# Optimization experiments

Hardware: AMD Instinct MI355X
Metric: run time of the kernel (lower is better)

Reference implementation:

```python
import jax, jax.numpy as jnp
import numpy as np

EPS = 1e-5
NEG = -1e9

def rmsnorm(x, g, eps=EPS):
    x32 = x.astype(jnp.float32)
    n = x32 * jax.lax.rsqrt(jnp.mean(x32 * x32, axis=-1, keepdims=True) + eps)
    return g * n.astype(x.dtype)

def setup_inputs() -> dict:
    key = jax.random.key(0)
    ks = jax.random.split(key, 10)
    B, S, D, H = 2, 2048, 768, 12
    F = 4 * D
    s = 0.02
    return {
        "x": jax.random.normal(ks[0], (B, S, D), jnp.float32),
        "mask": jax.random.randint(ks[1], (B, S, S), 0, 2, jnp.int32),
        "wq": jax.random.normal(ks[2], (D, D), jnp.float32) * s,
        "wk": jax.random.normal(ks[3], (D, D), jnp.float32) * s,
        "wv": jax.random.normal(ks[4], (D, D), jnp.float32) * s,
        "wo": jax.random.normal(ks[5], (D, D), jnp.float32) * s,
        "w1": jax.random.normal(ks[6], (F, D), jnp.float32) * s,
        "w2": jax.random.normal(ks[7], (D, F), jnp.float32) * s,
        "w3": jax.random.normal(ks[8], (F, D), jnp.float32) * s,
        "g_attn": jnp.ones((D,), jnp.float32),
        "g_ffn": jnp.ones((D,), jnp.float32),
    }

def reference(x, mask, wq, wk, wv, wo, w1, w2, w3, g_attn, g_ffn):
    B, S, D = x.shape
    H = 12
    Dk = D // H
    # --- attention sub-block (pre-norm) ---
    xn = rmsnorm(x, g_attn)
    # torch Linear: y = x @ W^T; split heads -> [B,H,S,Dk]
    q = (xn @ wq.T).reshape(B, S, H, Dk).transpose(0, 2, 1, 3)
    k = (xn @ wk.T).reshape(B, S, H, Dk).transpose(0, 2, 1, 3)
    v = (xn @ wv.T).reshape(B, S, H, Dk).transpose(0, 2, 1, 3)
    scores = jnp.einsum("bhqd,bhkd->bhqk", q, k) / jnp.sqrt(jnp.float32(Dk))
    scores = jnp.where(mask[:, None, :, :] == 0, jnp.float32(NEG), scores)
    probs = jax.nn.softmax(scores, axis=-1)  # dropout p=0.0 -> identity
    attn = jnp.einsum("bhqk,bhkd->bhqd", probs, v)
    attn = attn.transpose(0, 2, 1, 3).reshape(B, S, D)
    h = x + attn @ wo.T
    # --- SwiGLU FFN sub-block (pre-norm) ---
    hn = rmsnorm(h, g_ffn)
    ffn = (jax.nn.silu(hn @ w1.T) * (hn @ w3.T)) @ w2.T
    return h + ffn
```

## Files before the change

### kernel.cpp

```cpp
#include <hip/hip_runtime.h>
#include <hip/hip_bf16.h>

#define S_LEN 2048
#define D_MODEL 768
#define NH 12
#define DK 64
#define F_DIM 3072
#define BATCH 2
#define M_ROWS (BATCH * S_LEN)

typedef __bf16 bf16x8 __attribute__((ext_vector_type(8)));
typedef float floatx4 __attribute__((ext_vector_type(4)));
typedef unsigned short u16;
typedef unsigned long long u64;

__device__ inline float bf2f(u16 u) {
    union { unsigned int i; float f; } x; x.i = ((unsigned int)u) << 16; return x.f;
}
__device__ inline u16 f2bf(float f) {
    union { float f; unsigned int i; } x; x.f = f;
    unsigned int r = x.i + 0x7fffu + ((x.i >> 16) & 1u);
    return (u16)(r >> 16);
}

__device__ __forceinline__ void ldsload16(const u16* g, u16* l) {
    __builtin_amdgcn_global_load_lds(
        (const __attribute__((address_space(1))) unsigned int*)g,
        (__attribute__((address_space(3))) unsigned int*)l, 16, 0, 0);
}

__global__ __launch_bounds__(256)
void cvt_all(const float4* __restrict__ wq, const float4* __restrict__ wk,
             const float4* __restrict__ wv, const float4* __restrict__ wo,
             const float4* __restrict__ w1, const float4* __restrict__ w2,
             const float4* __restrict__ w3,
             ushort4* wqb, ushort4* wkb, ushort4* wvb, ushort4* wob,
             ushort4* w1b, ushort4* w2b, ushort4* w3b) {
    const int WS4 = (D_MODEL * D_MODEL) / 4;
    const int WB4 = (F_DIM * D_MODEL) / 4;
    int i = blockIdx.x * 256 + threadIdx.x;
    const float4* src; ushort4* dst; int off;
    if (i < 4 * WS4) {
        int s = i / WS4; off = i - s * WS4;
        src = (s == 0) ? wq : (s == 1) ? wk : (s == 2) ? wv : wo;
        dst = (s == 0) ? wqb : (s == 1) ? wkb : (s == 2) ? wvb : wob;
    } else {
        int j = i - 4 * WS4; int s = j / WB4; off = j - s * WB4;
        src = (s == 0) ? w1 : (s == 1) ? w2 : w3;
        dst = (s == 0) ? w1b : (s == 1) ? w2b : w3b;
    }
    float4 v = src[off];
    ushort4 o;
    o.x = f2bf(v.x); o.y = f2bf(v.y); o.z = f2bf(v.z); o.w = f2bf(v.w);
    dst[off] = o;
}

__global__ __launch_bounds__(256)
void mask_bits(const int* __restrict__ m, u64* __restrict__ bits) {
    size_t gid = (size_t)blockIdx.x * 256 + threadIdx.x;
    u64 b = __ballot(m[gid] != 0);
    if ((threadIdx.x & 63) == 0) bits[gid >> 6] = b;
}

__global__ __launch_bounds__(256)
void rmsnorm_k(const float* __restrict__ x, const float* __restrict__ g, u16* __restrict__ out) {
    int row = blockIdx.x;
    const float* xr = x + (size_t)row * D_MODEL;
    u16* orow = out + (size_t)row * D_MODEL;
    int t = threadIdx.x;
    float v0 = xr[t];
    float v1 = xr[t + 256];
    float v2 = xr[t + 512];
    float ss = v0 * v0 + v1 * v1 + v2 * v2;
    #pragma unroll
    for (int off = 1; off < 64; off <<= 1) ss += __shfl_xor(ss, off);
    __shared__ float red[4];
    if ((t & 63) == 0) red[t >> 6] = ss;
    __syncthreads();
    float tot = red[0] + red[1] + red[2] + red[3];
    float scale = rsqrtf(tot * (1.0f / (float)D_MODEL) + 1e-5f);
    orow[t]       = f2bf(g[t]       * v0 * scale);
    orow[t + 256] = f2bf(g[t + 256] * v1 * scale);
    orow[t + 512] = f2bf(g[t + 512] * v2 * scale);
}

template <int MODE, int MINW>
__global__ __launch_bounds__(256, MINW)
void gemm_t(const u16* __restrict__ A, const u16* __restrict__ B1,
            const u16* __restrict__ B2, const float* __restrict__ R,
            void* __restrict__ Cout, int N, int K) {
    __shared__ u16 As[2][64][32];
    __shared__ u16 Bs[2][128][32];
    __shared__ u16 Bs2[(MODE == 2) ? 2 : 1][(MODE == 2) ? 128 : 1][32];

    int t = threadIdx.x;
    int w = t >> 6, lane = t & 63;
    int mBase = blockIdx.y * 64, nBase = blockIdx.x * 128;
    int lrow = lane & 15, quad = lane >> 4;
    int wm = (w >> 1) * 32, wn = (w & 1) * 64;

    int srow = lane >> 2, scol = (lane & 3) * 8;
    const u16* Ag  = A  + (size_t)(mBase + w * 16 + srow) * K + scol;
    const u16* Bg  = B1 + (size_t)(nBase + w * 32 + srow) * K + scol;
    const u16* B2g = (MODE == 2) ? (B2 + (size_t)(nBase + w * 32 + srow) * K + scol) : nullptr;

    auto stage = [&](int k0, int b) {
        ldsload16(Ag + k0, &As[b][w * 16][0]);
        ldsload16(Bg + k0, &Bs[b][w * 32][0]);
        ldsload16(Bg + (size_t)16 * K + k0, &Bs[b][w * 32 + 16][0]);
        if (MODE == 2) {
            ldsload16(B2g + k0, &Bs2[b][w * 32][0]);
            ldsload16(B2g + (size_t)16 * K + k0, &Bs2[b][w * 32 + 16][0]);
        }
    };

    floatx4 zero = {0.f, 0.f, 0.f, 0.f};
    floatx4 acc[2][4], acc2[(MODE == 2) ? 2 : 1][(MODE == 2) ? 4 : 1];
    #pragma unroll
    for (int r = 0; r < 2; ++r)
        #pragma unroll
        for (int c = 0; c < 4; ++c) acc[r][c] = zero;
    if (MODE == 2)
        #pragma unroll
        for (int r = 0; r < 2; ++r)
            #pragma unroll
            for (int c = 0; c < 4; ++c) acc2[r][c] = zero;

    stage(0, 0);
    int cur = 0;
    for (int k0 = 0; k0 < K; k0 += 32) {
        __syncthreads();
        if (k0 + 32 < K) stage(k0 + 32, cur ^ 1);

        bf16x8 af[2];
        #pragma unroll
        for (int r = 0; r < 2; ++r) af[r] = *(const bf16x8*)&As[cur][wm + r * 16 + lrow][quad * 8];
        #pragma unroll
        for (int c = 0; c < 4; ++c) {
            bf16x8 bfr = *(const bf16x8*)&Bs[cur][wn + c * 16 + lrow][quad * 8];
            #pragma unroll
            for (int r = 0; r < 2; ++r)
                acc[r][c] = __builtin_amdgcn_mfma_f32_16x16x32_bf16(af[r], bfr, acc[r][c], 0, 0, 0);
            if (MODE == 2) {
                bf16x8 b2f = *(const bf16x8*)&Bs2[cur][wn + c * 16 + lrow][quad * 8];
                #pragma unroll
                for (int r = 0; r < 2; ++r)
                    acc2[r][c] = __builtin_amdgcn_mfma_f32_16x16x32_bf16(af[r], b2f, acc2[r][c], 0, 0, 0);
            }
        }
        cur ^= 1;
    }

    #pragma unroll
    for (int r = 0; r < 2; ++r) {
        #pragma unroll
        for (int c = 0; c < 4; ++c) {
            #pragma unroll
            for (int j = 0; j < 4; ++j) {
                int grow = mBase + wm + r * 16 + quad * 4 + j;
                int gcol = nBase + wn + c * 16 + lrow;
                size_t idx = (size_t)grow * N + gcol;
                float val = acc[r][c][j];
                if (MODE == 1) {
                    ((float*)Cout)[idx] = val + R[idx];
                } else {
                    float a = val;
                    ((u16*)Cout)[idx] = f2bf((a / (1.0f + __expf(-a))) * acc2[r][c][j]);
                }
            }
        }
    }
}

__global__ __launch_bounds__(256, 3)
void gemm64(const u16* __restrict__ A, const u16* __restrict__ B1,
            const float* __restrict__ R, float* __restrict__ Cout, int N, int K) {
    __shared__ u16 As[2][64][32];
    __shared__ u16 Bs[2][64][32];

    int t = threadIdx.x;
    int w = t >> 6, lane = t & 63;
    int mBase = blockIdx.y * 64, nBase = blockIdx.x * 64;
    int lrow = lane & 15, quad = lane >> 4;
    int wm = (w >> 1) * 32, wn = (w & 1) * 32;

    int srow = lane >> 2, scol = (lane & 3) * 8;
    const u16* Ag = A  + (size_t)(mBase + w * 16 + srow) * K + scol;
    const u16* Bg = B1 + (size_t)(nBase + w * 16 + srow) * K + scol;

    auto stage = [&](int k0, int b) {
        ldsload16(Ag + k0, &As[b][w * 16][0]);
        ldsload16(Bg + k0, &Bs[b][w * 16][0]);
    };

    floatx4 zero = {0.f, 0.f, 0.f, 0.f};
    floatx4 acc[2][2];
    #pragma unroll
    for (int r = 0; r < 2; ++r)
        #pragma unroll
        for (int c = 0; c < 2; ++c) acc[r][c] = zero;

    stage(0, 0);
    int cur = 0;
    for (int k0 = 0; k0 < K; k0 += 32) {
        __syncthreads();
        if (k0 + 32 < K) stage(k0 + 32, cur ^ 1);

        bf16x8 af[2], bf[2];
        #pragma unroll
        for (int r = 0; r < 2; ++r) af[r] = *(const bf16x8*)&As[cur][wm + r * 16 + lrow][quad * 8];
        #pragma unroll
        for (int c = 0; c < 2; ++c) bf[c] = *(const bf16x8*)&Bs[cur][wn + c * 16 + lrow][quad * 8];
        #pragma unroll
        for (int r = 0; r < 2; ++r)
            #pragma unroll
            for (int c = 0; c < 2; ++c)
                acc[r][c] = __builtin_amdgcn_mfma_f32_16x16x32_bf16(af[r], bf[c], acc[r][c], 0, 0, 0);
        cur ^= 1;
    }

    #pragma unroll
    for (int r = 0; r < 2; ++r) {
        #pragma unroll
        for (int c = 0; c < 2; ++c) {
            #pragma unroll
            for (int j = 0; j < 4; ++j) {
                int grow = mBase + wm + r * 16 + quad * 4 + j;
                int gcol = nBase + wn + c * 16 + lrow;
                size_t idx = (size_t)grow * N + gcol;
                Cout[idx] = acc[r][c][j] + R[idx];
            }
        }
    }
}

__global__ __launch_bounds__(256, 4)
void gemm_qkv(const u16* __restrict__ A, const u16* __restrict__ wq,
              const u16* __restrict__ wk, const u16* __restrict__ wv,
              u16* __restrict__ qb, u16* __restrict__ kb, u16* __restrict__ vt) {
    const int K = D_MODEL;
    __shared__ u16 As[2][64][32];
    __shared__ u16 Bs[2][128][32];

    int t = threadIdx.x;
    int w = t >> 6, lane = t & 63;
    int nb = blockIdx.x;
    int which = nb / 6;
    int mBase = blockIdx.y * 64, nBase = (nb % 6) * 128;
    const u16* B1 = (which == 0) ? wq : (which == 1) ? wk : wv;
    int lrow = lane & 15, quad = lane >> 4;
    int wm = (w >> 1) * 32, wn = (w & 1) * 64;

    int srow = lane >> 2, scol = (lane & 3) * 8;
    const u16* Ag = A  + (size_t)(mBase + w * 16 + srow) * K + scol;
    const u16* Bg = B1 + (size_t)(nBase + w * 32 + srow) * K + scol;

    auto stage = [&](int k0, int b) {
        ldsload16(Ag + k0, &As[b][w * 16][0]);
        ldsload16(Bg + k0, &Bs[b][w * 32][0]);
        ldsload16(Bg + (size_t)16 * K + k0, &Bs[b][w * 32 + 16][0]);
    };

    floatx4 zero = {0.f, 0.f, 0.f, 0.f};
    floatx4 acc[2][4];
    #pragma unroll
    for (int r = 0; r < 2; ++r)
        #pragma unroll
        for (int c = 0; c < 4; ++c) acc[r][c] = zero;

    stage(0, 0);
    int cur = 0;
    for (int k0 = 0; k0 < K; k0 += 32) {
        __syncthreads();
        if (k0 + 32 < K) stage(k0 + 32, cur ^ 1);
        bf16x8 af[2];
        #pragma unroll
        for (int r = 0; r < 2; ++r) af[r] = *(const bf16x8*)&As[cur][wm + r * 16 + lrow][quad * 8];
        #pragma unroll
        for (int c = 0; c < 4; ++c) {
            bf16x8 bfr = *(const bf16x8*)&Bs[cur][wn + c * 16 + lrow][quad * 8];
            #pragma unroll
            for (int r = 0; r < 2; ++r)
                acc[r][c] = __builtin_amdgcn_mfma_f32_16x16x32_bf16(af[r], bfr, acc[r][c], 0, 0, 0);
        }
        cur ^= 1;
    }

    u16* dst = (which == 0) ? qb : kb;
    const float qscale = 0.18033688011112042f;
    #pragma unroll
    for (int r = 0; r < 2; ++r) {
        #pragma unroll
        for (int c = 0; c < 4; ++c) {
            #pragma unroll
            for (int j = 0; j < 4; ++j) {
                int grow = mBase + wm + r * 16 + quad * 4 + j;
                int gcol = nBase + wn + c * 16 + lrow;
                float val = acc[r][c][j];
                if (which == 2) {
                    int bb = grow >> 11, s = grow & 2047;
                    int hh = gcol >> 6, d = gcol & 63;
                    vt[((((size_t)bb * NH + hh) * DK + d) << 11) + s] = f2bf(val);
                } else {
                    if (which == 0) val *= qscale;
                    dst[(size_t)grow * D_MODEL + gcol] = f2bf(val);
                }
            }
        }
    }
}

__global__ __launch_bounds__(256)
void attn_mfma(const u16* __restrict__ q, const u16* __restrict__ k,
               const u16* __restrict__ vt, const u64* __restrict__ mbits,
               u16* __restrict__ out) {
    __shared__ u16 Qs0[64][32], Qs1[64][32];
    __shared__ u16 Ks0[64][32], Ks1[64][32];
    __shared__ u16 Vs0[64][32], Vs1[64][32];
    __shared__ u16 PT[4][16][72];

    int t = threadIdx.x;
    int lane = t & 63;
    int w = t >> 6;
    int lrow = lane & 15;
    int quad = lane >> 4;

    int st0 = blockIdx.x * 64;
    int bh = blockIdx.y;
    int h = bh % NH;
    int b = bh / NH;

    const u16* qbase = q + ((size_t)b * S_LEN + st0) * D_MODEL + h * DK;
    const u16* kbase = k + (size_t)b * S_LEN * D_MODEL + h * DK;
    const u16* vbase = vt + (size_t)bh * DK * S_LEN;
    const u64* bw = mbits + ((size_t)b * S_LEN + st0 + w * 16 + lrow) * (S_LEN / 64);

    int srow = lane >> 2;
    int scol = (lane & 3) * 8;

    const u16* qg = qbase + (size_t)(w * 16 + srow) * D_MODEL + scol;
    ldsload16(qg, &Qs0[w * 16][0]);
    ldsload16(qg + 32, &Qs1[w * 16][0]);
    __syncthreads();
    bf16x8 bq0 = *(const bf16x8*)&Qs0[w * 16 + lrow][quad * 8];
    bf16x8 bq1 = *(const bf16x8*)&Qs1[w * 16 + lrow][quad * 8];

    const u16* kg = kbase + (size_t)(w * 16 + srow) * D_MODEL + scol;
    const u16* vg = vbase + (size_t)(w * 16 + srow) * S_LEN + scol;

    bf16x8 ones;
    {
        union { u16 u; __bf16 b; } o; o.u = 0x3F80;
        #pragma unroll
        for (int j = 0; j < 8; ++j) ones[j] = o.b;
    }

    floatx4 zero = {0.f, 0.f, 0.f, 0.f};
    floatx4 Ot[4] = {zero, zero, zero, zero};
    floatx4 Osum = zero;

    for (int kt = 0; kt < S_LEN; kt += 64) {
        u64 mw = bw[kt >> 6];
        unsigned mlo = (unsigned)mw, mhi = (unsigned)(mw >> 32);
        __syncthreads();
        ldsload16(kg + (size_t)kt * D_MODEL, &Ks0[w * 16][0]);
        ldsload16(kg + (size_t)kt * D_MODEL + 32, &Ks1[w * 16][0]);
        ldsload16(vg + kt, &Vs0[w * 16][0]);
        ldsload16(vg + kt + 32, &Vs1[w * 16][0]);
        __syncthreads();

        floatx4 st[4];
        #pragma unroll
        for (int nt = 0; nt < 4; ++nt) {
            bf16x8 ak0 = *(const bf16x8*)&Ks0[nt * 16 + lrow][quad * 8];
            bf16x8 ak1 = *(const bf16x8*)&Ks1[nt * 16 + lrow][quad * 8];
            st[nt] = __builtin_amdgcn_mfma_f32_16x16x32_bf16(ak0, bq0, zero, 0, 0, 0);
            st[nt] = __builtin_amdgcn_mfma_f32_16x16x32_bf16(ak1, bq1, st[nt], 0, 0, 0);
        }

        #pragma unroll
        for (int nt = 0; nt < 4; ++nt) {
            unsigned half = (nt & 2) ? mhi : mlo;
            unsigned tmp = half >> ((nt & 1) * 16 + quad * 4);
            unsigned eu[4];
            #pragma unroll
            for (int j = 0; j < 4; ++j) {
                float e = __builtin_amdgcn_exp2f(st[nt][j]);
                unsigned msk = (unsigned)((int)(tmp << (31 - j)) >> 31);
                eu[j] = __float_as_uint(e) & msk;
            }
            uint2 p;
            p.x = (eu[0] >> 16) | (eu[1] & 0xffff0000u);
            p.y = (eu[2] >> 16) | (eu[3] & 0xffff0000u);
            *(uint2*)&PT[w][lrow][nt * 16 + quad * 4] = p;
        }

        bf16x8 ap0 = *(const bf16x8*)&PT[w][lrow][quad * 8];
        bf16x8 ap1 = *(const bf16x8*)&PT[w][lrow][32 + quad * 8];
        Osum = __builtin_amdgcn_mfma_f32_16x16x32_bf16(ap0, ones, Osum, 0, 0, 0);
        Osum = __builtin_amdgcn_mfma_f32_16x16x32_bf16(ap1, ones, Osum, 0, 0, 0);
        #pragma unroll
        for (int dt = 0; dt < 4; ++dt) {
            bf16x8 bv0 = *(const bf16x8*)&Vs0[dt * 16 + lrow][quad * 8];
            bf16x8 bv1 = *(const bf16x8*)&Vs1[dt * 16 + lrow][quad * 8];
            Ot[dt] = __builtin_amdgcn_mfma_f32_16x16x32_bf16(ap0, bv0, Ot[dt], 0, 0, 0);
            Ot[dt] = __builtin_amdgcn_mfma_f32_16x16x32_bf16(ap1, bv1, Ot[dt], 0, 0, 0);
        }
    }

    float invj[4];
    #pragma unroll
    for (int j = 0; j < 4; ++j) invj[j] = 1.0f / Osum[j];

    u16* obase = out + ((size_t)b * S_LEN + st0 + w * 16) * D_MODEL + h * DK;
    #pragma unroll
    for (int dt = 0; dt < 4; ++dt)
        #pragma unroll
        for (int j = 0; j < 4; ++j)
            obase[(size_t)(quad * 4 + j) * D_MODEL + dt * 16 + lrow] = f2bf(Ot[dt][j] * invj[j]);
}

extern "C" void kernel_launch(void* const* d_in, const int* in_sizes, int n_in,
                              void* d_out, int out_size, void* d_ws, size_t ws_size,
                              hipStream_t stream) {
    const float* x      = (const float*)d_in[0];
    const int*   mask   = (const int*)d_in[1];
    const float* wq     = (const float*)d_in[2];
    const float* wk     = (const float*)d_in[3];
    const float* wv     = (const float*)d_in[4];
    const float* wo     = (const float*)d_in[5];
    const float* w1     = (const float*)d_in[6];
    const float* w2     = (const float*)d_in[7];
    const float* w3     = (const float*)d_in[8];
    const float* g_attn = (const float*)d_in[9];
    const float* g_ffn  = (const float*)d_in[10];
    float* out = (float*)d_out;

    const size_t WSMALL = (size_t)D_MODEL * D_MODEL;
    const size_t WBIG   = (size_t)F_DIM * D_MODEL;
    const size_t MD     = (size_t)M_ROWS * D_MODEL;

    char* ws = (char*)d_ws;
    u16* wqb = (u16*)ws;             ws += WSMALL * 2;
    u16* wkb = (u16*)ws;             ws += WSMALL * 2;
    u16* wvb = (u16*)ws;             ws += WSMALL * 2;
    u16* wob = (u16*)ws;             ws += WSMALL * 2;
    u16* w1b = (u16*)ws;             ws += WBIG * 2;
    u16* w2b = (u16*)ws;             ws += WBIG * 2;
    u16* w3b = (u16*)ws;             ws += WBIG * 2;
    u16* xn  = (u16*)ws;             ws += MD * 2;
    u16* qb  = (u16*)ws;             ws += MD * 2;
    u16* kb  = (u16*)ws;             ws += MD * 2;
    u16* vb  = (u16*)ws;             ws += MD * 2;
    u16* ao  = (u16*)ws;             ws += MD * 2;
    float* hb = (float*)ws;          ws += MD * 4;
    u64* mb  = (u64*)ws;             ws += (size_t)BATCH * S_LEN * (S_LEN / 64) * 8;
    u16* hn = xn;
    u16* ub = qb;
    (void)ws_size; (void)n_in; (void)in_sizes; (void)out_size;

    dim3 blk(256);

    cvt_all<<<9216, blk, 0, stream>>>((const float4*)wq, (const float4*)wk, (const float4*)wv,
                                      (const float4*)wo, (const float4*)w1, (const float4*)w2,
                                      (const float4*)w3,
                                      (ushort4*)wqb, (ushort4*)wkb, (ushort4*)wvb, (ushort4*)wob,
                                      (ushort4*)w1b, (ushort4*)w2b, (ushort4*)w3b);
    mask_bits<<<(BATCH * S_LEN * S_LEN) / 256, blk, 0, stream>>>(mask, mb);

    rmsnorm_k<<<M_ROWS, blk, 0, stream>>>(x, g_attn, xn);
    gemm_qkv<<<dim3(18, M_ROWS / 64), blk, 0, stream>>>(xn, wqb, wkb, wvb, qb, kb, vb);
    attn_mfma<<<dim3(S_LEN / 64, BATCH * NH), blk, 0, stream>>>(qb, kb, vb, mb, ao);
    gemm64<<<dim3(D_MODEL / 64, M_ROWS / 64), blk, 0, stream>>>(ao, wob, x, hb, D_MODEL, D_MODEL);
    rmsnorm_k<<<M_ROWS, blk, 0, stream>>>((const float*)hb, g_ffn, hn);
    gemm_t<2, 3><<<dim3(F_DIM / 128, M_ROWS / 64), blk, 0, stream>>>(hn, w1b, w3b, nullptr, ub, F_DIM, D_MODEL);
    gemm64<<<dim3(D_MODEL / 64, M_ROWS / 64), blk, 0, stream>>>(ub, w2b, hb, out, D_MODEL, F_DIM);
}
```

Measured before the change: 369.5 us.

## Interleave W1/W3 into one bf16 buffer and halve FFN1 gemm N-tile

Weight conversion now writes W1 and W3 rows interleaved in 64-row groups into a single buffer, so the fused SwiGLU gemm loads one 128-row B tile holding 64 gate rows and 64 up rows. The FFN1 kernel uses a 64x64 output tile per block instead of 64x128 with two separate B tiles, which cuts LDS use and accumulator registers and doubles the grid for better occupancy. In exchange, arithmetic intensity per block drops and A tiles are reloaded twice as often across the grid.

After: 377.8 us. 1.02x slower.

```diff
diff --git a/kernel.cpp b/kernel.cpp
--- a/kernel.cpp
+++ b/kernel.cpp
@@ -35,24 +35,31 @@
              const float4* __restrict__ w1, const float4* __restrict__ w2,
              const float4* __restrict__ w3,
              ushort4* wqb, ushort4* wkb, ushort4* wvb, ushort4* wob,
-             ushort4* w1b, ushort4* w2b, ushort4* w3b) {
+             ushort4* w13b, ushort4* w2b) {
     const int WS4 = (D_MODEL * D_MODEL) / 4;
     const int WB4 = (F_DIM * D_MODEL) / 4;
+    const int RW4 = D_MODEL / 4;
     int i = blockIdx.x * 256 + threadIdx.x;
-    const float4* src; ushort4* dst; int off;
+    const float4* src; ushort4* dst; int off, doff;
     if (i < 4 * WS4) {
-        int s = i / WS4; off = i - s * WS4;
+        int s = i / WS4; off = i - s * WS4; doff = off;
         src = (s == 0) ? wq : (s == 1) ? wk : (s == 2) ? wv : wo;
         dst = (s == 0) ? wqb : (s == 1) ? wkb : (s == 2) ? wvb : wob;
     } else {
         int j = i - 4 * WS4; int s = j / WB4; off = j - s * WB4;
-        src = (s == 0) ? w1 : (s == 1) ? w2 : w3;
-        dst = (s == 0) ? w1b : (s == 1) ? w2b : w3b;
+        if (s == 1) { src = w2; dst = w2b; doff = off; }
+        else {
+            src = (s == 0) ? w1 : w3;
+            dst = w13b;
+            int row = off / RW4, c4 = off - row * RW4;
+            int rp = (row >> 6) * 128 + (row & 63) + ((s == 0) ? 0 : 64);
+            doff = rp * RW4 + c4;
+        }
     }
     float4 v = src[off];
     ushort4 o;
     o.x = f2bf(v.x); o.y = f2bf(v.y); o.z = f2bf(v.z); o.w = f2bf(v.w);
-    dst[off] = o;
+    dst[doff] = o;
 }
 
 __global__ __launch_bounds__(256)
@@ -84,47 +91,35 @@
     orow[t + 512] = f2bf(g[t + 512] * v2 * scale);
 }
 
-template <int MODE, int MINW>
-__global__ __launch_bounds__(256, MINW)
-void gemm_t(const u16* __restrict__ A, const u16* __restrict__ B1,
-            const u16* __restrict__ B2, const float* __restrict__ R,
-            void* __restrict__ Cout, int N, int K) {
+__global__ __launch_bounds__(256, 3)
+void gemm_f1(const u16* __restrict__ A, const u16* __restrict__ W13,
+             u16* __restrict__ Cout) {
+    const int K = D_MODEL, N = F_DIM;
     __shared__ u16 As[2][64][32];
     __shared__ u16 Bs[2][128][32];
-    __shared__ u16 Bs2[(MODE == 2) ? 2 : 1][(MODE == 2) ? 128 : 1][32];
 
     int t = threadIdx.x;
     int w = t >> 6, lane = t & 63;
-    int mBase = blockIdx.y * 64, nBase = blockIdx.x * 128;
+    int mBase = blockIdx.y * 64, nBase = blockIdx.x * 64;
     int lrow = lane & 15, quad = lane >> 4;
-    int wm = (w >> 1) * 32, wn = (w & 1) * 64;
+    int wm = (w >> 1) * 32, wn = (w & 1) * 32;
 
     int srow = lane >> 2, scol = (lane & 3) * 8;
-    const u16* Ag  = A  + (size_t)(mBase + w * 16 + srow) * K + scol;
-    const u16* Bg  = B1 + (size_t)(nBase + w * 32 + srow) * K + scol;
-    const u16* B2g = (MODE == 2) ? (B2 + (size_t)(nBase + w * 32 + srow) * K + scol) : nullptr;
+    const u16* Ag = A   + (size_t)(mBase + w * 16 + srow) * K + scol;
+    const u16* Bg = W13 + (size_t)(blockIdx.x * 128 + w * 32 + srow) * K + scol;
 
     auto stage = [&](int k0, int b) {
         ldsload16(Ag + k0, &As[b][w * 16][0]);
         ldsload16(Bg + k0, &Bs[b][w * 32][0]);
         ldsload16(Bg + (size_t)16 * K + k0, &Bs[b][w * 32 + 16][0]);
-        if (MODE == 2) {
-            ldsload16(B2g + k0, &Bs2[b][w * 32][0]);
-            ldsload16(B2g + (size_t)16 * K + k0, &Bs2[b][w * 32 + 16][0]);
-        }
     };
 
     floatx4 zero = {0.f, 0.f, 0.f, 0.f};
-    floatx4 acc[2][4], acc2[(MODE == 2) ? 2 : 1][(MODE == 2) ? 4 : 1];
+    floatx4 acc[2][2], acc2[2][2];
     #pragma unroll
     for (int r = 0; r < 2; ++r)
         #pragma unroll
-        for (int c = 0; c < 4; ++c) acc[r][c] = zero;
-    if (MODE == 2)
-        #pragma unroll
-        for (int r = 0; r < 2; ++r)
-            #pragma unroll
-            for (int c = 0; c < 4; ++c) acc2[r][c] = zero;
+        for (int c = 0; c < 2; ++c) { acc[r][c] = zero; acc2[r][c] = zero; }
 
     stage(0, 0);
     int cur = 0;
@@ -132,41 +127,34 @@
         __syncthreads();
         if (k0 + 32 < K) stage(k0 + 32, cur ^ 1);
 
-        bf16x8 af[2];
+        bf16x8 af[2], b1f[2], b3f[2];
         #pragma unroll
         for (int r = 0; r < 2; ++r) af[r] = *(const bf16x8*)&As[cur][wm + r * 16 + lrow][quad * 8];
         #pragma unroll
-        for (int c = 0; c < 4; ++c) {
-            bf16x8 bfr = *(const bf16x8*)&Bs[cur][wn + c * 16 + lrow][quad * 8];
-            #pragma unroll
-            for (int r = 0; r < 2; ++r)
-                acc[r][c] = __builtin_amdgcn_mfma_f32_16x16x32_bf16(af[r], bfr, acc[r][c], 0, 0, 0);
-            if (MODE == 2) {
-                bf16x8 b2f = *(const bf16x8*)&Bs2[cur][wn + c * 16 + lrow][quad * 8];
-                #pragma unroll
-                for (int r = 0; r < 2; ++r)
-                    acc2[r][c] = __builtin_amdgcn_mfma_f32_16x16x32_bf16(af[r], b2f, acc2[r][c], 0, 0, 0);
+        for (int c = 0; c < 2; ++c) {
+            b1f[c] = *(const bf16x8*)&Bs[cur][wn + c * 16 + lrow][quad * 8];
+            b3f[c] = *(const bf16x8*)&Bs[cur][64 + wn + c * 16 + lrow][quad * 8];
+        }
+        #pragma unroll
+        for (int r = 0; r < 2; ++r)
+            #pragma unroll
+            for (int c = 0; c < 2; ++c) {
+                acc[r][c]  = __builtin_amdgcn_mfma_f32_16x16x32_bf16(af[r], b1f[c], acc[r][c], 0, 0, 0);
+                acc2[r][c] = __builtin_amdgcn_mfma_f32_16x16x32_bf16(af[r], b3f[c], acc2[r][c], 0, 0, 0);
             }
-        }
         cur ^= 1;
     }
 
     #pragma unroll
     for (int r = 0; r < 2; ++r) {
         #pragma unroll
-        for (int c = 0; c < 4; ++c) {
+        for (int c = 0; c < 2; ++c) {
             #pragma unroll
             for (int j = 0; j < 4; ++j) {
                 int grow = mBase + wm + r * 16 + quad * 4 + j;
                 int gcol = nBase + wn + c * 16 + lrow;
-                size_t idx = (size_t)grow * N + gcol;
-                float val = acc[r][c][j];
-                if (MODE == 1) {
-                    ((float*)Cout)[idx] = val + R[idx];
-                } else {
-                    float a = val;
-                    ((u16*)Cout)[idx] = f2bf((a / (1.0f + __expf(-a))) * acc2[r][c][j]);
-                }
+                float a = acc[r][c][j];
+                Cout[(size_t)grow * N + gcol] = f2bf((a / (1.0f + __expf(-a))) * acc2[r][c][j]);
             }
         }
     }
@@ -441,13 +429,12 @@
     const size_t MD     = (size_t)M_ROWS * D_MODEL;
 
     char* ws = (char*)d_ws;
-    u16* wqb = (u16*)ws;             ws += WSMALL * 2;
-    u16* wkb = (u16*)ws;             ws += WSMALL * 2;
-    u16* wvb = (u16*)ws;             ws += WSMALL * 2;
-    u16* wob = (u16*)ws;             ws += WSMALL * 2;
-    u16* w1b = (u16*)ws;             ws += WBIG * 2;
-    u16* w2b = (u16*)ws;             ws += WBIG * 2;
-    u16* w3b = (u16*)ws;             ws += WBIG * 2;
+    u16* wqb  = (u16*)ws;            ws += WSMALL * 2;
+    u16* wkb  = (u16*)ws;            ws += WSMALL * 2;
+    u16* wvb  = (u16*)ws;            ws += WSMALL * 2;
+    u16* wob  = (u16*)ws;            ws += WSMALL * 2;
+    u16* w13b = (u16*)ws;            ws += WBIG * 2 * 2;
+    u16* w2b  = (u16*)ws;            ws += WBIG * 2;
     u16* xn  = (u16*)ws;             ws += MD * 2;
     u16* qb  = (u16*)ws;             ws += MD * 2;
     u16* kb  = (u16*)ws;             ws += MD * 2;
@@ -465,7 +452,7 @@
                                       (const float4*)wo, (const float4*)w1, (const float4*)w2,
                                       (const float4*)w3,
                                       (ushort4*)wqb, (ushort4*)wkb, (ushort4*)wvb, (ushort4*)wob,
-                                      (ushort4*)w1b, (ushort4*)w2b, (ushort4*)w3b);
+                                      (ushort4*)w13b, (ushort4*)w2b);
     mask_bits<<<(BATCH * S_LEN * S_LEN) / 256, blk, 0, stream>>>(mask, mb);
 
     rmsnorm_k<<<M_ROWS, blk, 0, stream>>>(x, g_attn, xn);
@@ -473,6 +460,6 @@
     attn_mfma<<<dim3(S_LEN / 64, BATCH * NH), blk, 0, stream>>>(qb, kb, vb, mb, ao);
     gemm64<<<dim3(D_MODEL / 64, M_ROWS / 64), blk, 0, stream>>>(ao, wob, x, hb, D_MODEL, D_MODEL);
     rmsnorm_k<<<M_ROWS, blk, 0, stream>>>((const float*)hb, g_ffn, hn);
-    gemm_t<2, 3><<<dim3(F_DIM / 128, M_ROWS / 64), blk, 0, stream>>>(hn, w1b, w3b, nullptr, ub, F_DIM, D_MODEL);
+    gemm_f1<<<dim3(F_DIM / 64, M_ROWS / 64), blk, 0, stream>>>(hn, w13b, ub);
     gemm64<<<dim3(D_MODEL / 64, M_ROWS / 64), blk, 0, stream>>>(ub, w2b, hb, out, D_MODEL, F_DIM);
 }
```
